# Performance work log

Measured on AMD Instinct MI355X. Metric: run time of the kernel, lower is better.

## Reference

```python
import math
import jax, jax.numpy as jnp
import numpy as np

# MLA dims (DeepSeek-style, scaled)
B, S, H = 1, 2048, 2048
NH = 16            # num attention heads
DN = 128           # qk_nope_head_dim
DR = 64            # qk_rope_head_dim
DV = 128           # v_head_dim
QL = 1536          # q_lora_rank
KL = 512           # kv_lora_rank
EPS = 1e-6         # rms_norm_eps
ROPE_BASE = 10000.0


def setup_inputs() -> dict:
    key = jax.random.key(0)
    ks = jax.random.split(key, 6)
    w = 0.02  # weight init scale to keep activations sane
    return {
        "hidden": jax.random.normal(ks[0], (B, S, H), jnp.float32),
        "w_kv_a": jax.random.normal(ks[1], (H, QL + KL + DR), jnp.float32) * w,
        "q_a_gamma": jnp.ones((QL,), jnp.float32),
        "w_qb": jax.random.normal(ks[2], (QL, NH * (DN + DR)), jnp.float32) * w,
        "kv_a_gamma": jnp.ones((KL,), jnp.float32),
        "w_kvb": jax.random.normal(ks[3], (KL, NH * (DN + DV)), jnp.float32) * w,
        "w_o": jax.random.normal(ks[4], (NH * DV, H), jnp.float32) * w,
    }


def _rmsnorm(x, gamma, eps=EPS):
    return x * gamma * jax.lax.rsqrt(jnp.mean(x * x, axis=-1, keepdims=True) + eps)


def _rope_tables(seq_len, dim, dtype):
    inv_freq = 1.0 / (ROPE_BASE ** (jnp.arange(0, dim, 2, dtype=jnp.float32) / dim))
    ang = jnp.arange(seq_len, dtype=jnp.float32)[:, None] * inv_freq  # [S, dim/2]
    cos = jnp.concatenate([jnp.cos(ang)] * 2, axis=-1).astype(dtype)  # [S, dim]
    sin = jnp.concatenate([jnp.sin(ang)] * 2, axis=-1).astype(dtype)
    return cos[None, :, None, :], sin[None, :, None, :]  # broadcast to [B,S,h,dim]


def _rotate_half(x):
    h = x.shape[-1] // 2
    return jnp.concatenate([-x[..., h:], x[..., :h]], axis=-1)


def reference(hidden, w_kv_a, q_a_gamma, w_qb, kv_a_gamma, w_kvb, w_o):
    b, s, _ = hidden.shape
    # Fused down-projection: [compressed_q | compressed_kv | k_rope]
    fused = hidden @ w_kv_a                          # [B,S,QL+KL+DR]
    q_c = fused[..., :QL]
    kv_c = fused[..., QL:QL + KL]
    k_pe = fused[..., QL + KL:]                      # [B,S,DR], shared across heads (MQA rope)

    # Q up-projection from normalized latent
    q = _rmsnorm(q_c, q_a_gamma) @ w_qb              # [B,S,NH*(DN+DR)]
    q = q.reshape(b, s, NH, DN + DR)
    q_nope, q_pe = q[..., :DN], q[..., DN:]

    # KV up-projection from normalized latent
    kv = _rmsnorm(kv_c, kv_a_gamma) @ w_kvb          # [B,S,NH*(DN+DV)]
    kv = kv.reshape(b, s, NH, DN + DV)
    k_nope, v = kv[..., :DN], kv[..., DN:]

    # RoPE on the rope slices only
    cos, sin = _rope_tables(s, DR, hidden.dtype)
    q_pe = q_pe * cos + _rotate_half(q_pe) * sin     # [B,S,NH,DR]
    k_pe = k_pe[:, :, None, :]
    k_pe = k_pe * cos + _rotate_half(k_pe) * sin     # [B,S,1,DR]

    q_full = jnp.concatenate([q_nope, q_pe], axis=-1)                         # [B,S,NH,DN+DR]
    k_full = jnp.concatenate([k_nope, jnp.broadcast_to(k_pe, (b, s, NH, DR))], axis=-1)

    scale = 1.0 / math.sqrt(DN + DR)
    scores = jnp.einsum('bqhd,bkhd->bhqk', q_full, k_full) * scale            # [B,NH,S,S]
    pos = jnp.arange(s)
    causal = pos[:, None] >= pos[None, :]
    scores = jnp.where(causal[None, None], scores, jnp.asarray(-1e30, scores.dtype))
    probs = jax.nn.softmax(scores, axis=-1)
    attn = jnp.einsum('bhqk,bkhd->bqhd', probs, v)                            # [B,S,NH,DV]
    return attn.reshape(b, s, NH * DV) @ w_o                                  # [B,S,H]
```

## Files before the change

kernel.cpp:

```cpp
#include <hip/hip_runtime.h>
#include <math.h>

#define S_LEN 2048
#define NH 16
#define DN 128
#define DR 64
#define DV 128
#define QL 1536
#define KL 512
#define FUSED_N 2112
#define FPAD 2176
#define QB_N 3072
#define KVB_N 4096
#define HD_QK 192
#define EPS_RMS 1e-6f

typedef _Float16 f16;
typedef _Float16 half8 __attribute__((ext_vector_type(8)));
typedef _Float16 half4 __attribute__((ext_vector_type(4)));
typedef float floatx4 __attribute__((ext_vector_type(4)));

__global__ __launch_bounds__(256) void cvt_f16_k(const float* __restrict__ in,
                                                 f16* __restrict__ out, int n4)
{
    int i = blockIdx.x * 256 + threadIdx.x;
    if (i < n4) {
        float4 v = ((const float4*)in)[i];
        half4 h;
        h[0] = (f16)v.x; h[1] = (f16)v.y; h[2] = (f16)v.z; h[3] = (f16)v.w;
        ((half4*)out)[i] = h;
    }
}

__global__ __launch_bounds__(256) void tconv_k(const float* __restrict__ in,
                                               f16* __restrict__ out,
                                               int K, int N)
{
    __shared__ float t[32][33];
    const int k0 = blockIdx.y * 32, n0 = blockIdx.x * 32;
    const int c = threadIdx.x & 31, r8 = threadIdx.x >> 5;
    #pragma unroll
    for (int i = 0; i < 4; ++i) {
        int r = r8 + i * 8;
        int gc = n0 + c;
        t[r][c] = (gc < N) ? in[(size_t)(k0 + r) * N + gc] : 0.f;
    }
    __syncthreads();
    #pragma unroll
    for (int i = 0; i < 4; ++i) {
        int r = r8 + i * 8;
        out[(size_t)(n0 + r) * K + k0 + c] = (f16)t[c][r];
    }
}

__device__ __forceinline__ void async16(const f16* gp, f16* lp)
{
    __builtin_amdgcn_global_load_lds(
        (const __attribute__((address_space(1))) void*)gp,
        (__attribute__((address_space(3))) void*)lp, 16, 0, 0);
}

template <int OUT_F16>
__global__ __launch_bounds__(256) void gemm_mfma(
    const f16* __restrict__ A,
    const f16* __restrict__ Bt,
    void* __restrict__ Cv, int M, int N, int K)
{
    __shared__ f16 As[128 * 64];
    __shared__ f16 Bs[128 * 64];

    const int tid = threadIdx.x;
    const int wv = tid >> 6, lane = tid & 63;
    const int quad = lane >> 4, l15 = lane & 15;
    const int wr = wv >> 1, wc = wv & 1;
    const int bm = blockIdx.y * 128, bn = blockIdx.x * 128;
    const int srow = lane >> 3;
    const int sc = lane & 7;

    floatx4 acc[4][4] = {};

    for (int k0 = 0; k0 < K; k0 += 64) {
        #pragma unroll
        for (int t = 0; t < 4; ++t) {
            int rl = wv * 32 + t * 8 + srow;
            int ch = sc ^ (rl & 7);
            async16(A  + (size_t)(bm + rl) * K + k0 + ch * 8,
                    &As[(wv * 32 + t * 8) * 64]);
            async16(Bt + (size_t)(bn + rl) * K + k0 + ch * 8,
                    &Bs[(wv * 32 + t * 8) * 64]);
        }
        __syncthreads();

        #pragma unroll
        for (int ks = 0; ks < 2; ++ks) {
            half8 av[4], bv[4];
            #pragma unroll
            for (int i = 0; i < 4; ++i) {
                int m = wr * 64 + i * 16 + l15;
                av[i] = *(const half8*)&As[m * 64 + ((ks * 4 + quad) ^ (m & 7)) * 8];
            }
            #pragma unroll
            for (int j = 0; j < 4; ++j) {
                int n = wc * 64 + j * 16 + l15;
                bv[j] = *(const half8*)&Bs[n * 64 + ((ks * 4 + quad) ^ (n & 7)) * 8];
            }
            #pragma unroll
            for (int i = 0; i < 4; ++i)
                #pragma unroll
                for (int j = 0; j < 4; ++j)
                    acc[i][j] = __builtin_amdgcn_mfma_f32_16x16x32_f16(
                        av[i], bv[j], acc[i][j], 0, 0, 0);
        }
        __syncthreads();
    }

    #pragma unroll
    for (int i = 0; i < 4; ++i) {
        int rbase = bm + wr * 64 + i * 16 + quad * 4;
        #pragma unroll
        for (int j = 0; j < 4; ++j) {
            int cidx = bn + wc * 64 + j * 16 + l15;
            #pragma unroll
            for (int rr = 0; rr < 4; ++rr) {
                if (OUT_F16)
                    ((f16*)Cv)[(size_t)(rbase + rr) * N + cidx] = (f16)acc[i][j][rr];
                else
                    ((float*)Cv)[(size_t)(rbase + rr) * N + cidx] = acc[i][j][rr];
            }
        }
    }
}

__global__ __launch_bounds__(256) void rmsnorm_k(
    const float* __restrict__ in, int stride, int ncols,
    const float* __restrict__ gamma, f16* __restrict__ out)
{
    const int row = blockIdx.x;
    const float* x = in + (size_t)row * stride;

    float ss = 0.f;
    for (int c = threadIdx.x; c < ncols; c += 256) {
        float v = x[c];
        ss += v * v;
    }
    #pragma unroll
    for (int off = 32; off > 0; off >>= 1) ss += __shfl_down(ss, off);

    __shared__ float warp_s[4];
    __shared__ float scale_s;
    const int wid = threadIdx.x >> 6;
    if ((threadIdx.x & 63) == 0) warp_s[wid] = ss;
    __syncthreads();
    if (threadIdx.x == 0) {
        float t = warp_s[0] + warp_s[1] + warp_s[2] + warp_s[3];
        scale_s = rsqrtf(t / (float)ncols + EPS_RMS);
    }
    __syncthreads();
    const float sc = scale_s;
    for (int c = threadIdx.x; c < ncols; c += 256)
        out[(size_t)row * ncols + c] = (f16)(x[c] * gamma[c] * sc);
}

__device__ __forceinline__ float rope_one(int s, int d, float x, float other)
{
    const int j = d & 31;
    const float invf = expf(-0.28782313662425572f * (float)j);
    const float ang = (float)s * invf;
    float sn, cs;
    sincosf(ang, &sn, &cs);
    float rot = (d < 32) ? -other : other;
    return x * cs + rot * sn;
}

__global__ __launch_bounds__(256) void rope_q_k(f16* __restrict__ q)
{
    const int s = blockIdx.x;
    const int h = blockIdx.y * 4 + (threadIdx.x >> 6);
    const int d = threadIdx.x & 63;
    f16* base = q + (size_t)s * QB_N + h * HD_QK + DN;
    float x = (float)base[d];
    float other = (float)((d < 32) ? base[d + 32] : base[d - 32]);
    base[d] = (f16)rope_one(s, d, x, other);
}

__global__ void rope_kpe_k(const float* __restrict__ fused, f16* __restrict__ kpe)
{
    const int s = blockIdx.x, d = threadIdx.x;
    const float* src = fused + (size_t)s * FPAD + (QL + KL);
    float x = src[d];
    float other = (d < 32) ? src[d + 32] : src[d - 32];
    kpe[(size_t)s * DR + d] = (f16)rope_one(s, d, x, other);
}

__global__ __launch_bounds__(256) void kfull_k(const f16* __restrict__ kv,
                                               const f16* __restrict__ kpe,
                                               f16* __restrict__ kfull)
{
    int n = blockIdx.x * 256 + threadIdx.x;
    int c8 = n % 24;
    int s = (n / 24) & 2047;
    int h = n / (24 * 2048);
    half8 v;
    if (c8 < 16)
        v = *(const half8*)&kv[(size_t)s * KVB_N + h * 256 + c8 * 8];
    else
        v = *(const half8*)&kpe[(size_t)s * DR + (c8 - 16) * 8];
    *(half8*)&kfull[((size_t)h * S_LEN + s) * HD_QK + c8 * 8] = v;
}

__global__ __launch_bounds__(256) void vt_k(const f16* __restrict__ kv,
                                            f16* __restrict__ vt)
{
    __shared__ f16 t[32][33];
    const int s0 = blockIdx.x * 32, d0 = blockIdx.y * 32, h = blockIdx.z;
    const int tid = threadIdx.x;
    {
        const int c = tid & 31, rb = tid >> 5;
        #pragma unroll
        for (int i = 0; i < 4; ++i) {
            int r = rb + i * 8;
            t[r][c] = kv[(size_t)(s0 + r) * KVB_N + h * 256 + 128 + d0 + c];
        }
    }
    __syncthreads();
    {
        const int d = tid >> 3, s4 = tid & 7;
        half4 v;
        v[0] = t[s4 * 4 + 0][d];
        v[1] = t[s4 * 4 + 1][d];
        v[2] = t[s4 * 4 + 2][d];
        v[3] = t[s4 * 4 + 3][d];
        *(half4*)&vt[((size_t)h * DV + d0 + d) * S_LEN + s0 + s4 * 4] = v;
    }
}

__global__ __launch_bounds__(256) void attn_mfma_k(
    const f16* __restrict__ q,
    const f16* __restrict__ kfull,
    const f16* __restrict__ vt,
    f16* __restrict__ attn)
{
    __shared__ f16 sm[25088];

    const int tid = threadIdx.x;
    const int w = tid >> 6, lane = tid & 63;
    const int quad = lane >> 4, l15 = lane & 15;
    const int wbase = w * 64;
    const int h = blockIdx.y;
    const int qb = (blockIdx.y < 8) ? (int)blockIdx.x : 31 - (int)blockIdx.x;
    const int q0 = qb * 64;
    const float scale2 = 0.10411755f;

    const f16* kf_h = kfull + (size_t)h * S_LEN * HD_QK;
    const f16* vt_h = vt + (size_t)h * DV * S_LEN;

    int koff[3];
    #pragma unroll
    for (int j = 0; j < 3; ++j) {
        int sig = j * 256 + tid;
        int r = sig / 24, cs = sig - r * 24;
        int ch = (cs & 24) | ((cs & 7) ^ (r & 7));
        koff[j] = r * HD_QK + ch * 8;
    }
    int voff[2];
    #pragma unroll
    for (int j = 0; j < 2; ++j) {
        int sig = j * 256 + tid;
        int rv = sig >> 2, c = (sig & 3) ^ ((rv >> 1) & 3);
        voff[j] = rv * S_LEN + c * 8;
    }

    #pragma unroll
    for (int j = 0; j < 6; ++j) {
        int sig = j * 256 + tid;
        int r = sig / 24, cs = sig - r * 24;
        int ch = (cs & 24) | ((cs & 7) ^ (r & 7));
        async16(q + (size_t)(q0 + r) * QB_N + h * HD_QK + ch * 8,
                sm + 10240 + (j * 256 + wbase) * 8);
    }
    #pragma unroll
    for (int j = 0; j < 3; ++j) async16(kf_h + koff[j], sm + (j * 256 + wbase) * 8);
    #pragma unroll
    for (int j = 0; j < 2; ++j) async16(vt_h + voff[j], sm + 6144 + (j * 256 + wbase) * 8);
    __syncthreads();

    half8 qf[6];
    const int qrow = w * 16 + l15;
    #pragma unroll
    for (int kd = 0; kd < 6; ++kd) {
        int c = kd * 4 + quad;
        int cs = (c & 24) | ((c & 7) ^ (qrow & 7));
        qf[kd] = *(const half8*)&sm[10240 + (qrow * 24 + cs) * 8];
    }

    floatx4 o[8] = {};
    float m_i[4], l_i[4];
    #pragma unroll
    for (int r = 0; r < 4; ++r) { m_i[r] = -1e30f; l_i[r] = 0.f; }

    const int qrow_min = q0 + w * 16;
    const int ntiles = q0 / 32 + 2;
    f16* Pw = sm + 22528 + w * 640;

    for (int kt = 0; kt < ntiles; ++kt) {
        const int cur = kt & 1;
        __syncthreads();
        if (kt + 1 < ntiles) {
            const int nxt = 1 - cur;
            const int k0n = (kt + 1) * 32;
            f16* kb = sm + (nxt ? 10240 : 0);
            f16* vb = sm + (nxt ? 16384 : 6144);
            const f16* kg = kf_h + (size_t)k0n * HD_QK;
            const f16* vg = vt_h + k0n;
            #pragma unroll
            for (int j = 0; j < 3; ++j) async16(kg + koff[j], kb + (j * 256 + wbase) * 8);
            #pragma unroll
            for (int j = 0; j < 2; ++j) async16(vg + voff[j], vb + (j * 256 + wbase) * 8);
        }
        const int k0 = kt * 32;
        if (k0 > qrow_min + 15) continue;

        const f16* kb = sm + (cur ? 10240 : 0);
        const f16* vb = sm + (cur ? 16384 : 6144);

        floatx4 s0 = {}, s1 = {};
        #pragma unroll
        for (int kd = 0; kd < 6; ++kd) {
            int c = kd * 4 + quad;
            int cs = (c & 24) | ((c & 7) ^ (l15 & 7));
            half8 b0 = *(const half8*)&kb[(l15 * 24 + cs) * 8];
            half8 b1 = *(const half8*)&kb[((l15 + 16) * 24 + cs) * 8];
            s0 = __builtin_amdgcn_mfma_f32_16x16x32_f16(qf[kd], b0, s0, 0, 0, 0);
            s1 = __builtin_amdgcn_mfma_f32_16x16x32_f16(qf[kd], b1, s1, 0, 0, 0);
        }

        const bool nm = (k0 + 31 > qrow_min);
        float mt[4];
        #pragma unroll
        for (int r = 0; r < 4; ++r) {
            float v0 = s0[r] * scale2, v1 = s1[r] * scale2;
            if (nm) {
                int row = qrow_min + quad * 4 + r;
                if (k0 + l15 > row)      v0 = -1e30f;
                if (k0 + 16 + l15 > row) v1 = -1e30f;
            }
            s0[r] = v0; s1[r] = v1;
            mt[r] = fmaxf(v0, v1);
        }
        #pragma unroll
        for (int r = 0; r < 4; ++r) {
            mt[r] = fmaxf(mt[r], __shfl_xor(mt[r], 1));
            mt[r] = fmaxf(mt[r], __shfl_xor(mt[r], 2));
            mt[r] = fmaxf(mt[r], __shfl_xor(mt[r], 4));
            mt[r] = fmaxf(mt[r], __shfl_xor(mt[r], 8));
        }
        float alpha[4], ps[4];
        #pragma unroll
        for (int r = 0; r < 4; ++r) {
            float mn = fmaxf(m_i[r], mt[r]);
            alpha[r] = __builtin_exp2f(m_i[r] - mn);
            m_i[r] = mn;
            float p0 = __builtin_exp2f(s0[r] - mn);
            float p1 = __builtin_exp2f(s1[r] - mn);
            s0[r] = p0; s1[r] = p1;
            ps[r] = p0 + p1;
        }
        #pragma unroll
        for (int r = 0; r < 4; ++r) {
            ps[r] += __shfl_xor(ps[r], 1);
            ps[r] += __shfl_xor(ps[r], 2);
            ps[r] += __shfl_xor(ps[r], 4);
            ps[r] += __shfl_xor(ps[r], 8);
            l_i[r] = l_i[r] * alpha[r] + ps[r];
        }

        #pragma unroll
        for (int r = 0; r < 4; ++r) {
            Pw[(quad * 4 + r) * 40 + l15]      = (f16)s0[r];
            Pw[(quad * 4 + r) * 40 + 16 + l15] = (f16)s1[r];
        }

        #pragma unroll
        for (int nb = 0; nb < 8; ++nb)
            #pragma unroll
            for (int r = 0; r < 4; ++r) o[nb][r] *= alpha[r];

        half8 pa = *(const half8*)&Pw[l15 * 40 + quad * 8];
        #pragma unroll
        for (int nb = 0; nb < 8; ++nb) {
            int rv = nb * 16 + l15;
            int sig = rv * 4 + (quad ^ ((l15 >> 1) & 3));
            half8 vv = *(const half8*)&vb[sig * 8];
            o[nb] = __builtin_amdgcn_mfma_f32_16x16x32_f16(pa, vv, o[nb], 0, 0, 0);
        }
    }

    float inv[4];
    #pragma unroll
    for (int r = 0; r < 4; ++r) inv[r] = 1.f / l_i[r];
    #pragma unroll
    for (int nb = 0; nb < 8; ++nb) {
        #pragma unroll
        for (int r = 0; r < 4; ++r) {
            int row = q0 + w * 16 + quad * 4 + r;
            attn[(size_t)row * (NH * DV) + h * DV + nb * 16 + l15] =
                (f16)(o[nb][r] * inv[r]);
        }
    }
}

extern "C" void kernel_launch(void* const* d_in, const int* in_sizes, int n_in,
                              void* d_out, int out_size, void* d_ws, size_t ws_size,
                              hipStream_t stream)
{
    const float* hidden   = (const float*)d_in[0];
    const float* w_kv_a   = (const float*)d_in[1];
    const float* q_gamma  = (const float*)d_in[2];
    const float* w_qb     = (const float*)d_in[3];
    const float* kv_gamma = (const float*)d_in[4];
    const float* w_kvb    = (const float*)d_in[5];
    const float* w_o      = (const float*)d_in[6];
    float* out = (float*)d_out;

    char* p = (char*)d_ws;
    f16* hid_h   = (f16*)p;  p += (size_t)2048 * 2048 * 2;
    f16* wkva_t  = (f16*)p;  p += (size_t)2176 * 2048 * 2;
    f16* wqb_t   = (f16*)p;  p += (size_t)3072 * 1536 * 2;
    f16* wkvb_t  = (f16*)p;  p += (size_t)4096 * 512 * 2;
    f16* wo_t    = (f16*)p;  p += (size_t)2048 * 2048 * 2;
    float* fused = (float*)p; p += (size_t)2048 * FPAD * 4;
    f16* q_n     = (f16*)p;  p += (size_t)2048 * QL * 2;
    f16* qbuf    = (f16*)p;  p += (size_t)2048 * QB_N * 2;
    f16* kv_n    = (f16*)p;  p += (size_t)2048 * KL * 2;
    f16* kvbuf   = (f16*)p;  p += (size_t)2048 * KVB_N * 2;
    f16* kpe     = (f16*)p;  p += (size_t)2048 * DR * 2;
    f16* attnb   = (f16*)p;  p += (size_t)2048 * 2048 * 2;

    f16* kfull = hid_h;
    f16* vt    = (f16*)fused;

    dim3 blk(256);

    cvt_f16_k<<<(2048 * 2048 / 4 + 255) / 256, blk, 0, stream>>>(hidden, hid_h, 2048 * 2048 / 4);
    tconv_k<<<dim3(2176 / 32, 2048 / 32), blk, 0, stream>>>(w_kv_a, wkva_t, 2048, FUSED_N);
    tconv_k<<<dim3(3072 / 32, 1536 / 32), blk, 0, stream>>>(w_qb,   wqb_t,  1536, QB_N);
    tconv_k<<<dim3(4096 / 32,  512 / 32), blk, 0, stream>>>(w_kvb,  wkvb_t,  512, KVB_N);
    tconv_k<<<dim3(2048 / 32, 2048 / 32), blk, 0, stream>>>(w_o,    wo_t,   2048, 2048);

    gemm_mfma<0><<<dim3(FPAD / 128, 2048 / 128), blk, 0, stream>>>(
        hid_h, wkva_t, fused, 2048, FPAD, 2048);

    rmsnorm_k<<<2048, blk, 0, stream>>>(fused, FPAD, QL, q_gamma, q_n);
    rmsnorm_k<<<2048, blk, 0, stream>>>(fused + QL, FPAD, KL, kv_gamma, kv_n);

    gemm_mfma<1><<<dim3(QB_N / 128, 2048 / 128), blk, 0, stream>>>(
        q_n, wqb_t, qbuf, 2048, QB_N, QL);
    gemm_mfma<1><<<dim3(KVB_N / 128, 2048 / 128), blk, 0, stream>>>(
        kv_n, wkvb_t, kvbuf, 2048, KVB_N, KL);

    rope_q_k<<<dim3(2048, 4), blk, 0, stream>>>(qbuf);
    rope_kpe_k<<<2048, dim3(64), 0, stream>>>(fused, kpe);

    kfull_k<<<16 * 2048 * 24 / 256, blk, 0, stream>>>(kvbuf, kpe, kfull);
    vt_k<<<dim3(2048 / 32, 128 / 32, NH), blk, 0, stream>>>(kvbuf, vt);

    attn_mfma_k<<<dim3(2048 / 64, NH), blk, 0, stream>>>(qbuf, kfull, vt, attnb);

    gemm_mfma<0><<<dim3(2048 / 128, 2048 / 128), blk, 0, stream>>>(
        attnb, wo_t, out, 2048, 2048, 2048);
}
```

Before: 402.8 us.

## Split attention KV range across two blocks and merge partials with combine kernel

```diff
diff --git a/kernel.cpp b/kernel.cpp
--- a/kernel.cpp
+++ b/kernel.cpp
@@ -183,17 +183,8 @@
     base[d] = (f16)rope_one(s, d, x, other);
 }
 
-__global__ void rope_kpe_k(const float* __restrict__ fused, f16* __restrict__ kpe)
-{
-    const int s = blockIdx.x, d = threadIdx.x;
-    const float* src = fused + (size_t)s * FPAD + (QL + KL);
-    float x = src[d];
-    float other = (d < 32) ? src[d + 32] : src[d - 32];
-    kpe[(size_t)s * DR + d] = (f16)rope_one(s, d, x, other);
-}
-
 __global__ __launch_bounds__(256) void kfull_k(const f16* __restrict__ kv,
-                                               const f16* __restrict__ kpe,
+                                               const float* __restrict__ fused,
                                                f16* __restrict__ kfull)
 {
     int n = blockIdx.x * 256 + threadIdx.x;
@@ -201,10 +192,19 @@
     int s = (n / 24) & 2047;
     int h = n / (24 * 2048);
     half8 v;
-    if (c8 < 16)
+    if (c8 < 16) {
         v = *(const half8*)&kv[(size_t)s * KVB_N + h * 256 + c8 * 8];
-    else
-        v = *(const half8*)&kpe[(size_t)s * DR + (c8 - 16) * 8];
+    } else {
+        const float* src = fused + (size_t)s * FPAD + (QL + KL);
+        int dbase = (c8 - 16) * 8;
+        #pragma unroll
+        for (int j = 0; j < 8; ++j) {
+            int d = dbase + j;
+            float x = src[d];
+            float other = src[(d < 32) ? d + 32 : d - 32];
+            v[j] = (f16)rope_one(s, d, x, other);
+        }
+    }
     *(half8*)&kfull[((size_t)h * S_LEN + s) * HD_QK + c8 * 8] = v;
 }
 
@@ -238,7 +238,8 @@
     const f16* __restrict__ q,
     const f16* __restrict__ kfull,
     const f16* __restrict__ vt,
-    f16* __restrict__ attn)
+    f16* __restrict__ part_o,
+    float* __restrict__ part_ml)
 {
     __shared__ f16 sm[25088];
 
@@ -247,8 +248,11 @@
     const int quad = lane >> 4, l15 = lane & 15;
     const int wbase = w * 64;
     const int h = blockIdx.y;
+    const int z = blockIdx.z;
     const int qb = (blockIdx.y < 8) ? (int)blockIdx.x : 31 - (int)blockIdx.x;
     const int q0 = qb * 64;
+    const int kt_begin = z ? (qb + 1) : 0;
+    const int kt_end   = z ? (2 * qb + 2) : (qb + 1);
     const float scale2 = 0.10411755f;
 
     const f16* kf_h = kfull + (size_t)h * S_LEN * HD_QK;
@@ -278,10 +282,14 @@
         async16(q + (size_t)(q0 + r) * QB_N + h * HD_QK + ch * 8,
                 sm + 10240 + (j * 256 + wbase) * 8);
     }
-    #pragma unroll
-    for (int j = 0; j < 3; ++j) async16(kf_h + koff[j], sm + (j * 256 + wbase) * 8);
-    #pragma unroll
-    for (int j = 0; j < 2; ++j) async16(vt_h + voff[j], sm + 6144 + (j * 256 + wbase) * 8);
+    {
+        const f16* kg = kf_h + (size_t)kt_begin * 32 * HD_QK;
+        const f16* vg = vt_h + kt_begin * 32;
+        #pragma unroll
+        for (int j = 0; j < 3; ++j) async16(kg + koff[j], sm + (j * 256 + wbase) * 8);
+        #pragma unroll
+        for (int j = 0; j < 2; ++j) async16(vg + voff[j], sm + 6144 + (j * 256 + wbase) * 8);
+    }
     __syncthreads();
 
     half8 qf[6];
@@ -293,19 +301,23 @@
         qf[kd] = *(const half8*)&sm[10240 + (qrow * 24 + cs) * 8];
     }
 
+    half8 ones_h;
+    #pragma unroll
+    for (int j = 0; j < 8; ++j) ones_h[j] = (f16)1.0f;
+
     floatx4 o[8] = {};
-    float m_i[4], l_i[4];
-    #pragma unroll
-    for (int r = 0; r < 4; ++r) { m_i[r] = -1e30f; l_i[r] = 0.f; }
+    floatx4 o_l = {};
+    float m_i[4];
+    #pragma unroll
+    for (int r = 0; r < 4; ++r) m_i[r] = -1e30f;
 
     const int qrow_min = q0 + w * 16;
-    const int ntiles = q0 / 32 + 2;
     f16* Pw = sm + 22528 + w * 640;
 
-    for (int kt = 0; kt < ntiles; ++kt) {
-        const int cur = kt & 1;
+    for (int kt = kt_begin; kt < kt_end; ++kt) {
+        const int cur = (kt - kt_begin) & 1;
         __syncthreads();
-        if (kt + 1 < ntiles) {
+        if (kt + 1 < kt_end) {
             const int nxt = 1 - cur;
             const int k0n = (kt + 1) * 32;
             f16* kb = sm + (nxt ? 10240 : 0);
@@ -354,24 +366,14 @@
             mt[r] = fmaxf(mt[r], __shfl_xor(mt[r], 4));
             mt[r] = fmaxf(mt[r], __shfl_xor(mt[r], 8));
         }
-        float alpha[4], ps[4];
+        float alpha[4];
         #pragma unroll
         for (int r = 0; r < 4; ++r) {
             float mn = fmaxf(m_i[r], mt[r]);
             alpha[r] = __builtin_exp2f(m_i[r] - mn);
             m_i[r] = mn;
-            float p0 = __builtin_exp2f(s0[r] - mn);
-            float p1 = __builtin_exp2f(s1[r] - mn);
-            s0[r] = p0; s1[r] = p1;
-            ps[r] = p0 + p1;
-        }
-        #pragma unroll
-        for (int r = 0; r < 4; ++r) {
-            ps[r] += __shfl_xor(ps[r], 1);
-            ps[r] += __shfl_xor(ps[r], 2);
-            ps[r] += __shfl_xor(ps[r], 4);
-            ps[r] += __shfl_xor(ps[r], 8);
-            l_i[r] = l_i[r] * alpha[r] + ps[r];
+            s0[r] = __builtin_exp2f(s0[r] - mn);
+            s1[r] = __builtin_exp2f(s1[r] - mn);
         }
 
         #pragma unroll
@@ -384,8 +386,11 @@
         for (int nb = 0; nb < 8; ++nb)
             #pragma unroll
             for (int r = 0; r < 4; ++r) o[nb][r] *= alpha[r];
+        #pragma unroll
+        for (int r = 0; r < 4; ++r) o_l[r] *= alpha[r];
 
         half8 pa = *(const half8*)&Pw[l15 * 40 + quad * 8];
+        o_l = __builtin_amdgcn_mfma_f32_16x16x32_f16(pa, ones_h, o_l, 0, 0, 0);
         #pragma unroll
         for (int nb = 0; nb < 8; ++nb) {
             int rv = nb * 16 + l15;
@@ -397,16 +402,52 @@
 
     float inv[4];
     #pragma unroll
-    for (int r = 0; r < 4; ++r) inv[r] = 1.f / l_i[r];
+    for (int r = 0; r < 4; ++r) inv[r] = (o_l[r] > 0.f) ? 1.f / o_l[r] : 0.f;
+
+    f16* po = part_o + (size_t)z * S_LEN * 2048;
     #pragma unroll
     for (int nb = 0; nb < 8; ++nb) {
         #pragma unroll
         for (int r = 0; r < 4; ++r) {
             int row = q0 + w * 16 + quad * 4 + r;
-            attn[(size_t)row * (NH * DV) + h * DV + nb * 16 + l15] =
+            po[(size_t)row * (NH * DV) + h * DV + nb * 16 + l15] =
                 (f16)(o[nb][r] * inv[r]);
         }
     }
+    if (l15 == 0) {
+        #pragma unroll
+        for (int r = 0; r < 4; ++r) {
+            int row = q0 + w * 16 + quad * 4 + r;
+            float* ml = part_ml + (((size_t)z * NH + h) * S_LEN + row) * 2;
+            ml[0] = m_i[r];
+            ml[1] = o_l[r];
+        }
+    }
+}
+
+__global__ __launch_bounds__(256) void attn_comb_k(
+    const f16* __restrict__ part_o, const float* __restrict__ part_ml,
+    f16* __restrict__ attnb)
+{
+    int g = blockIdx.x * 256 + threadIdx.x;
+    int h = (g >> 4) & 15;
+    int s = g >> 8;
+    const float* ml0 = part_ml + ((size_t)h * S_LEN + s) * 2;
+    const float* ml1 = part_ml + (((size_t)NH + h) * S_LEN + s) * 2;
+    float m0 = ml0[0], l0 = ml0[1];
+    float m1 = ml1[0], l1 = ml1[1];
+    float M = fmaxf(m0, m1);
+    float w0 = l0 * __builtin_exp2f(m0 - M);
+    float w1 = l1 * __builtin_exp2f(m1 - M);
+    float inv = 1.f / (w0 + w1);
+    w0 *= inv; w1 *= inv;
+    half8 p0 = *(const half8*)&part_o[(size_t)g * 8];
+    half8 p1 = *(const half8*)&part_o[(size_t)(524288 + g) * 8];
+    half8 r;
+    #pragma unroll
+    for (int j = 0; j < 8; ++j)
+        r[j] = (f16)(w0 * (float)p0[j] + w1 * (float)p1[j]);
+    *(half8*)&attnb[(size_t)g * 8] = r;
 }
 
 extern "C" void kernel_launch(void* const* d_in, const int* in_sizes, int n_in,
@@ -433,8 +474,9 @@
     f16* qbuf    = (f16*)p;  p += (size_t)2048 * QB_N * 2;
     f16* kv_n    = (f16*)p;  p += (size_t)2048 * KL * 2;
     f16* kvbuf   = (f16*)p;  p += (size_t)2048 * KVB_N * 2;
-    f16* kpe     = (f16*)p;  p += (size_t)2048 * DR * 2;
     f16* attnb   = (f16*)p;  p += (size_t)2048 * 2048 * 2;
+    f16* part_o  = (f16*)p;  p += (size_t)2 * 2048 * 2048 * 2;
+    float* part_ml = (float*)p; p += (size_t)2 * NH * 2048 * 2 * 4;
 
     f16* kfull = hid_h;
     f16* vt    = (f16*)fused;
@@ -459,12 +501,12 @@
         kv_n, wkvb_t, kvbuf, 2048, KVB_N, KL);
 
     rope_q_k<<<dim3(2048, 4), blk, 0, stream>>>(qbuf);
-    rope_kpe_k<<<2048, dim3(64), 0, stream>>>(fused, kpe);
-
-    kfull_k<<<16 * 2048 * 24 / 256, blk, 0, stream>>>(kvbuf, kpe, kfull);
+
+    kfull_k<<<16 * 2048 * 24 / 256, blk, 0, stream>>>(kvbuf, fused, kfull);
     vt_k<<<dim3(2048 / 32, 128 / 32, NH), blk, 0, stream>>>(kvbuf, vt);
 
-    attn_mfma_k<<<dim3(2048 / 64, NH), blk, 0, stream>>>(qbuf, kfull, vt, attnb);
+    attn_mfma_k<<<dim3(32, NH, 2), blk, 0, stream>>>(qbuf, kfull, vt, part_o, part_ml);
+    attn_comb_k<<<2048, blk, 0, stream>>>(part_o, part_ml, attnb);
 
     gemm_mfma<0><<<dim3(2048 / 128, 2048 / 128), blk, 0, stream>>>(
         attnb, wo_t, out, 2048, 2048, 2048);
```

After: 391.8 us. 2.7% less time.
